# Kernel tuning notes

Hardware: AMD Instinct MI355X
Metric: run time of the kernel (lower is better)

The kernel has to match this reference:

```python
import jax, jax.numpy as jnp
import numpy as np
import math

BLOCK = 8
N_COEFF = BLOCK * BLOCK  # 64
N_SAMPLE = 250
SEED = 0  # args.seed

# zigzag order: flat index m*8+n from the hardcoded loc table
ZIGZAG = jnp.array([
    0, 1, 8, 16, 9, 2, 3, 10, 17, 24, 32, 25, 18, 11, 4, 5,
    12, 19, 26, 33, 40, 48, 41, 34, 27, 20, 13, 6, 7, 14, 21, 28,
    35, 42, 49, 56, 57, 50, 43, 36, 29, 22, 15, 23, 30, 37, 44, 51,
    58, 59, 52, 45, 38, 31, 39, 46, 53, 60, 61, 54, 47, 55, 62, 63
], dtype=jnp.int32)


def dct_matrix():
    Q = np.zeros((BLOCK, BLOCK), dtype=np.float32)
    Q[0, :] = math.sqrt(1.0 / BLOCK)
    for i in range(1, BLOCK):
        for j in range(BLOCK):
            Q[i, j] = math.sqrt(2.0 / BLOCK) * math.cos((2 * j + 1) * math.pi * i / (2.0 * BLOCK))
    return jnp.asarray(Q)


def setup_inputs() -> dict:
    key = jax.random.key(0)
    x = jax.random.uniform(key, (64, 3, 512, 512), dtype=jnp.float32)
    return {"x": x}


def reference(x):
    Q = dct_matrix()
    # rgb -> ycbcr, luminance channel only (module discards Cb/Cr)
    x255 = x * 255.0
    y = (0.299 * x255[:, 0] + 0.587 * x255[:, 1] + 0.114 * x255[:, 2]) / 255.0  # [B,H,W]
    B, H, W = y.shape
    a, b = H // BLOCK, W // BLOCK
    # split into 8x8 blocks: [B, a, b, 8, 8]
    blocks = y.reshape(B, a, BLOCK, b, BLOCK).transpose(0, 1, 3, 2, 4)
    # per-block 2D DCT: Q @ block @ Q^T, batched as one einsum
    dct = jnp.einsum('ij,nabjk,lk->nabil', Q, blocks, Q)  # [B,a,b,8,8]
    image_dct_result = dct.transpose(0, 1, 3, 2, 4).reshape(B, 1, H, W)
    # zigzag gather over flattened block coefficients -> [B, 64, a*b]
    dist = dct.reshape(B, a * b, N_COEFF)[:, :, ZIGZAG].transpose(0, 2, 1)
    # per (sample, coefficient) random permutation sampling of 250 blocks
    keys = jax.random.split(jax.random.key(SEED), B * N_COEFF)
    idx = jax.vmap(lambda k: jax.random.permutation(k, a * b)[:N_SAMPLE])(keys)
    idx = idx.reshape(B, N_COEFF, N_SAMPLE)
    dct_coeff_sample = jnp.take_along_axis(dist, idx, axis=2)  # [B,64,250]
    return image_dct_result, dct_coeff_sample
```

## Files before the change

kernel.cpp:

```cpp
#include <hip/hip_runtime.h>
#include <hip/hip_bf16.h>
#include <cstdint>


#define BATCH 64
#define HW 512
#define NBLK 4096
#define NSAMPLE 250
#define IMG_ELEMS (HW * HW)

#define A0 0.35355339059327373f
#define A1 0.49039264020161522f
#define A2 0.46193976625564337f
#define A3 0.41573480615127262f
#define A4 0.35355339059327379f
#define A5 0.27778511650980111f
#define A6 0.19134171618254492f
#define A7 0.09754516100806412f

__constant__ float Qc[8][8] = {
    { A0,  A0,  A0,  A0,  A0,  A0,  A0,  A0},
    { A1,  A3,  A5,  A7, -A7, -A5, -A3, -A1},
    { A2,  A6, -A6, -A2, -A2, -A6,  A6,  A2},
    { A3, -A7, -A1, -A5,  A5,  A1,  A7, -A3},
    { A4, -A4, -A4,  A4,  A4, -A4, -A4,  A4},
    { A5, -A1,  A7,  A3, -A3, -A7,  A1, -A5},
    { A6, -A2,  A2, -A6, -A6,  A2, -A2,  A6},
    { A7, -A5,  A3, -A1,  A1, -A3,  A5, -A7},
};

__constant__ int ZIGZAG[64] = {
    0, 1, 8, 16, 9, 2, 3, 10, 17, 24, 32, 25, 18, 11, 4, 5,
    12, 19, 26, 33, 40, 48, 41, 34, 27, 20, 13, 6, 7, 14, 21, 28,
    35, 42, 49, 56, 57, 50, 43, 36, 29, 22, 15, 23, 30, 37, 44, 51,
    58, 59, 52, 45, 38, 31, 39, 46, 53, 60, 61, 54, 47, 55, 62, 63
};

__global__ __launch_bounds__(256) void dct_kernel(const float* __restrict__ x,
                                                  float* __restrict__ out) {
    __shared__ float ylds[8 * 8 * 32];

    const int t = threadIdx.x;
    const int wg = blockIdx.x;
    const int b = wg >> 7;
    const int ai = (wg >> 1) & 63;
    const int h = wg & 1;
    const int row0 = ai * 8;
    const int colbase = h * 256;

    {
        const int k = t >> 5;
        const int cg = t & 31;
        size_t off = (size_t)b * 3 * IMG_ELEMS + (size_t)(row0 + k) * HW +
                     colbase + cg * 8;
        float4 r0 = *(const float4*)(x + off);
        float4 r1 = *(const float4*)(x + off + 4);
        float4 g0 = *(const float4*)(x + off + IMG_ELEMS);
        float4 g1 = *(const float4*)(x + off + IMG_ELEMS + 4);
        float4 b0 = *(const float4*)(x + off + 2 * IMG_ELEMS);
        float4 b1 = *(const float4*)(x + off + 2 * IMG_ELEMS + 4);
        float R[8] = {r0.x, r0.y, r0.z, r0.w, r1.x, r1.y, r1.z, r1.w};
        float G[8] = {g0.x, g0.y, g0.z, g0.w, g1.x, g1.y, g1.z, g1.w};
        float B[8] = {b0.x, b0.y, b0.z, b0.w, b1.x, b1.y, b1.z, b1.w};
#pragma unroll
        for (int jj = 0; jj < 8; ++jj) {
            float y = (0.299f * (R[jj] * 255.0f) + 0.587f * (G[jj] * 255.0f) +
                       0.114f * (B[jj] * 255.0f)) / 255.0f;
            ylds[k * 256 + jj * 32 + cg] = y;
        }
    }
    __syncthreads();

    const int i = t >> 5;
    const int bi = t & 31;
    float qrow[8];
#pragma unroll
    for (int k = 0; k < 8; ++k) qrow[k] = Qc[i][k];

    float acc[8];
#pragma unroll
    for (int j = 0; j < 8; ++j) acc[j] = 0.0f;
#pragma unroll
    for (int k = 0; k < 8; ++k) {
#pragma unroll
        for (int j = 0; j < 8; ++j)
            acc[j] += qrow[k] * ylds[k * 256 + j * 32 + bi];
    }

    float d[8];
#pragma unroll
    for (int j = 0; j < 8; ++j) {
        float s = 0.0f;
#pragma unroll
        for (int k = 0; k < 8; ++k) s += acc[k] * Qc[j][k];
        d[j] = s;
    }
    float4* o = (float4*)(out + (size_t)b * IMG_ELEMS +
                          (size_t)(row0 + i) * HW + colbase + bi * 8);
    o[0] = make_float4(d[0], d[1], d[2], d[3]);
    o[1] = make_float4(d[4], d[5], d[6], d[7]);
}

__device__ __forceinline__ uint32_t rotl32(uint32_t v, int d) {
    return (v << d) | (v >> (32 - d));
}

__device__ __forceinline__ void tf2x32(uint32_t k0, uint32_t k1,
                                       uint32_t x0, uint32_t x1,
                                       uint32_t& o0, uint32_t& o1) {
    uint32_t ks0 = k0, ks1 = k1, ks2 = k0 ^ k1 ^ 0x1BD11BDAu;
    x0 += ks0; x1 += ks1;
#define TF_R(r) { x0 += x1; x1 = rotl32(x1, r); x1 ^= x0; }
    TF_R(13) TF_R(15) TF_R(26) TF_R(6)
    x0 += ks1; x1 += ks2 + 1u;
    TF_R(17) TF_R(29) TF_R(16) TF_R(24)
    x0 += ks2; x1 += ks0 + 2u;
    TF_R(13) TF_R(15) TF_R(26) TF_R(6)
    x0 += ks0; x1 += ks1 + 3u;
    TF_R(17) TF_R(29) TF_R(16) TF_R(24)
    x0 += ks1; x1 += ks2 + 4u;
    TF_R(13) TF_R(15) TF_R(26) TF_R(6)
    x0 += ks2; x1 += ks0 + 5u;
#undef TF_R
    o0 = x0; o1 = x1;
}

__device__ __forceinline__ void build4096(
    uint32_t s0, uint32_t s1,
    uint32_t* __restrict__ pack32, uint32_t* __restrict__ hist32,
    int tid, int w, int lane, uint32_t* __restrict__ wsum) {
    uint16_t* hist16 = (uint16_t*)hist32;

    __syncthreads();
#pragma unroll
    for (int q = 0; q < 4; ++q) hist32[tid + q * 512] = 0u;
    uint32_t keys[8];
#pragma unroll
    for (int e = 0; e < 8; ++e) {
        uint32_t o0, o1;
        tf2x32(s0, s1, 0u, (uint32_t)(tid + e * 512), o0, o1);
        keys[e] = o0 ^ o1;
    }
    __syncthreads();

    uint32_t ord[8];
#pragma unroll
    for (int e = 0; e < 8; ++e) {
        uint32_t bkt = keys[e] >> 20;
        uint32_t sh = (bkt & 1) << 4;
        uint32_t old = atomicAdd(&hist32[bkt >> 1], 1u << sh);
        ord[e] = (old >> sh) & 0xFFFFu;
    }
    __syncthreads();

    uint4 wv = ((const uint4*)hist32)[tid];
    uint32_t c0 = wv.x & 0xFFFFu, c1 = wv.x >> 16;
    uint32_t c2 = wv.y & 0xFFFFu, c3 = wv.y >> 16;
    uint32_t c4 = wv.z & 0xFFFFu, c5 = wv.z >> 16;
    uint32_t c6 = wv.w & 0xFFFFu, c7 = wv.w >> 16;
    uint32_t ssum = c0 + c1 + c2 + c3 + c4 + c5 + c6 + c7;
    uint32_t sc = ssum;
#pragma unroll
    for (int off = 1; off < 64; off <<= 1) {
        uint32_t t = __shfl_up(sc, off);
        if (lane >= off) sc += t;
    }
    if (lane == 63) wsum[w] = sc;
    __syncthreads();
    uint32_t ex = sc - ssum;
    for (int ww = 0; ww < w; ++ww) ex += wsum[ww];
    uint32_t p1 = ex + c0, p2 = p1 + c1, p3 = p2 + c2, p4 = p3 + c3;
    uint32_t p5 = p4 + c4, p6 = p5 + c5, p7 = p6 + c6, p8 = p7 + c7;
    uint4 ov;
    ov.x = p1 | (p2 << 16); ov.y = p3 | (p4 << 16);
    ov.z = p5 | (p6 << 16); ov.w = p7 | (p8 << 16);
    ((uint4*)hist32)[tid] = ov;
    __syncthreads();

#pragma unroll
    for (int e = 0; e < 8; ++e) {
        uint32_t bkt = keys[e] >> 20;
        uint32_t start = bkt ? (uint32_t)hist16[bkt - 1] : 0u;
        pack32[start + ord[e]] =
            ((keys[e] & 0xFFFFFu) << 12) | (uint32_t)(tid + e * 512);
    }
}

__device__ __forceinline__ uint32_t select4096(
    const uint16_t* __restrict__ hist16, const uint32_t* __restrict__ pack32,
    uint32_t s) {
    uint32_t lo = 0, hi = 4095;
#pragma unroll
    for (int it = 0; it < 12; ++it) {
        uint32_t mid = (lo + hi) >> 1;
        if ((uint32_t)hist16[mid] > s) hi = mid; else lo = mid + 1;
    }
    uint32_t b = lo;
    uint32_t start = b ? (uint32_t)hist16[b - 1] : 0u;
    uint32_t L = (uint32_t)hist16[b] - start;
    uint32_t c = pack32[start];
    if (L > 1) {
        uint32_t k = s - start;
        for (uint32_t cand = 0; cand < L; ++cand) {
            uint32_t cc = pack32[start + cand];
            uint32_t cnt = 0;
            for (uint32_t o = 0; o < L; ++o)
                cnt += (pack32[start + o] < cc) ? 1u : 0u;
            if (cnt == k) { c = cc; break; }
        }
    }
    return c & 0xFFFu;
}

__global__ __launch_bounds__(512) void sample_kernel(const float* __restrict__ img,
                                                     float* __restrict__ out2) {
    __shared__ __align__(16) uint32_t pack32[NBLK];
    __shared__ __align__(16) uint32_t hist32[2048];
    __shared__ uint16_t jsel[256];
    __shared__ uint32_t wsum[8];
    uint16_t* hist16 = (uint16_t*)hist32;

    const int tid = threadIdx.x;
    const int w = tid >> 6;
    const int lane = tid & 63;
    const int gb = blockIdx.x;

    uint32_t k0, k1, n0, n1, sA0, sA1, sB0, sB1;
    tf2x32(0u, 0u, 0u, (uint32_t)gb, k0, k1);
    tf2x32(k0, k1, 0u, 0u, n0, n1);
    tf2x32(k0, k1, 0u, 1u, sA0, sA1);
    tf2x32(n0, n1, 0u, 1u, sB0, sB1);

    build4096(sB0, sB1, pack32, hist32, tid, w, lane, wsum);
    __syncthreads();
    if (tid < NSAMPLE)
        jsel[tid] = (uint16_t)select4096(hist16, pack32, (uint32_t)tid);

    build4096(sA0, sA1, pack32, hist32, tid, w, lane, wsum);
    __syncthreads();

    int b = gb >> 6, c = gb & 63;
    int z = ZIGZAG[c];
    int i0z = z >> 3, j0z = z & 7;
    if (tid < NSAMPLE) {
        uint32_t i = select4096(hist16, pack32, (uint32_t)jsel[tid]);
        int ai = (int)i >> 6, bi = (int)i & 63;
        out2[(size_t)gb * NSAMPLE + tid] =
            img[(size_t)b * IMG_ELEMS + (size_t)(ai * 8 + i0z) * HW +
                (bi * 8 + j0z)];
    }
}

extern "C" void kernel_launch(void* const* d_in, const int* in_sizes, int n_in,
                              void* d_out, int out_size, void* d_ws, size_t ws_size,
                              hipStream_t stream) {
    const float* x = (const float*)d_in[0];
    float* out = (float*)d_out;
    dct_kernel<<<BATCH * 128, 256, 0, stream>>>(x, out);
    sample_kernel<<<BATCH * 64, 512, 0, stream>>>(out, out + (size_t)BATCH * IMG_ELEMS);
}
```

Measured before the change: 392.0 us.

## Interleave DCT and permutation-index work in one kernel, gather samples afterward

The DCT work and the random-permutation index computation now run side by side in one launch: odd workgroups do two DCT tiles each and even workgroups do the sampling-index build. Sampled indices go to a workspace buffer, and a small gather kernel then reads the DCT output. The point is to overlap the memory-bound DCT with the compute-bound Threefry/sort work, so the index generation no longer waits for the DCT to finish. In exchange it adds a workspace round trip and a third dependent step, and the DCT blocks carry a larger shared-memory footprint.

```diff
diff --git a/kernel.cpp b/kernel.cpp
--- a/kernel.cpp
+++ b/kernel.cpp
@@ -35,71 +35,6 @@
     35, 42, 49, 56, 57, 50, 43, 36, 29, 22, 15, 23, 30, 37, 44, 51,
     58, 59, 52, 45, 38, 31, 39, 46, 53, 60, 61, 54, 47, 55, 62, 63
 };
-
-__global__ __launch_bounds__(256) void dct_kernel(const float* __restrict__ x,
-                                                  float* __restrict__ out) {
-    __shared__ float ylds[8 * 8 * 32];
-
-    const int t = threadIdx.x;
-    const int wg = blockIdx.x;
-    const int b = wg >> 7;
-    const int ai = (wg >> 1) & 63;
-    const int h = wg & 1;
-    const int row0 = ai * 8;
-    const int colbase = h * 256;
-
-    {
-        const int k = t >> 5;
-        const int cg = t & 31;
-        size_t off = (size_t)b * 3 * IMG_ELEMS + (size_t)(row0 + k) * HW +
-                     colbase + cg * 8;
-        float4 r0 = *(const float4*)(x + off);
-        float4 r1 = *(const float4*)(x + off + 4);
-        float4 g0 = *(const float4*)(x + off + IMG_ELEMS);
-        float4 g1 = *(const float4*)(x + off + IMG_ELEMS + 4);
-        float4 b0 = *(const float4*)(x + off + 2 * IMG_ELEMS);
-        float4 b1 = *(const float4*)(x + off + 2 * IMG_ELEMS + 4);
-        float R[8] = {r0.x, r0.y, r0.z, r0.w, r1.x, r1.y, r1.z, r1.w};
-        float G[8] = {g0.x, g0.y, g0.z, g0.w, g1.x, g1.y, g1.z, g1.w};
-        float B[8] = {b0.x, b0.y, b0.z, b0.w, b1.x, b1.y, b1.z, b1.w};
-#pragma unroll
-        for (int jj = 0; jj < 8; ++jj) {
-            float y = (0.299f * (R[jj] * 255.0f) + 0.587f * (G[jj] * 255.0f) +
-                       0.114f * (B[jj] * 255.0f)) / 255.0f;
-            ylds[k * 256 + jj * 32 + cg] = y;
-        }
-    }
-    __syncthreads();
-
-    const int i = t >> 5;
-    const int bi = t & 31;
-    float qrow[8];
-#pragma unroll
-    for (int k = 0; k < 8; ++k) qrow[k] = Qc[i][k];
-
-    float acc[8];
-#pragma unroll
-    for (int j = 0; j < 8; ++j) acc[j] = 0.0f;
-#pragma unroll
-    for (int k = 0; k < 8; ++k) {
-#pragma unroll
-        for (int j = 0; j < 8; ++j)
-            acc[j] += qrow[k] * ylds[k * 256 + j * 32 + bi];
-    }
-
-    float d[8];
-#pragma unroll
-    for (int j = 0; j < 8; ++j) {
-        float s = 0.0f;
-#pragma unroll
-        for (int k = 0; k < 8; ++k) s += acc[k] * Qc[j][k];
-        d[j] = s;
-    }
-    float4* o = (float4*)(out + (size_t)b * IMG_ELEMS +
-                          (size_t)(row0 + i) * HW + colbase + bi * 8);
-    o[0] = make_float4(d[0], d[1], d[2], d[3]);
-    o[1] = make_float4(d[4], d[5], d[6], d[7]);
-}
 
 __device__ __forceinline__ uint32_t rotl32(uint32_t v, int d) {
     return (v << d) | (v >> (32 - d));
@@ -212,43 +147,119 @@
     return c & 0xFFFu;
 }
 
-__global__ __launch_bounds__(512) void sample_kernel(const float* __restrict__ img,
-                                                     float* __restrict__ out2) {
-    __shared__ __align__(16) uint32_t pack32[NBLK];
-    __shared__ __align__(16) uint32_t hist32[2048];
-    __shared__ uint16_t jsel[256];
+__global__ __launch_bounds__(512) void fused_kernel(const float* __restrict__ x,
+                                                    float* __restrict__ out,
+                                                    uint32_t* __restrict__ ws) {
+    __shared__ __align__(16) uint8_t smem[25088];
     __shared__ uint32_t wsum[8];
-    uint16_t* hist16 = (uint16_t*)hist32;
 
     const int tid = threadIdx.x;
-    const int w = tid >> 6;
-    const int lane = tid & 63;
+
+    if (blockIdx.x & 1) {
+        float* ylds = (float*)smem + (tid >> 8) * 2048;
+        const int t = tid & 255;
+        const int wg = ((int)blockIdx.x & ~1) | (tid >> 8);
+        const int b = wg >> 7;
+        const int ai = (wg >> 1) & 63;
+        const int h = wg & 1;
+        const int row0 = ai * 8;
+        const int colbase = h * 256;
+
+        {
+            const int k = t >> 5;
+            const int cg = t & 31;
+            size_t off = (size_t)b * 3 * IMG_ELEMS + (size_t)(row0 + k) * HW +
+                         colbase + cg * 8;
+            float4 r0 = *(const float4*)(x + off);
+            float4 r1 = *(const float4*)(x + off + 4);
+            float4 g0 = *(const float4*)(x + off + IMG_ELEMS);
+            float4 g1 = *(const float4*)(x + off + IMG_ELEMS + 4);
+            float4 b0 = *(const float4*)(x + off + 2 * IMG_ELEMS);
+            float4 b1 = *(const float4*)(x + off + 2 * IMG_ELEMS + 4);
+            float R[8] = {r0.x, r0.y, r0.z, r0.w, r1.x, r1.y, r1.z, r1.w};
+            float G[8] = {g0.x, g0.y, g0.z, g0.w, g1.x, g1.y, g1.z, g1.w};
+            float B[8] = {b0.x, b0.y, b0.z, b0.w, b1.x, b1.y, b1.z, b1.w};
+#pragma unroll
+            for (int jj = 0; jj < 8; ++jj) {
+                float y = (0.299f * (R[jj] * 255.0f) + 0.587f * (G[jj] * 255.0f) +
+                           0.114f * (B[jj] * 255.0f)) / 255.0f;
+                ylds[k * 256 + jj * 32 + cg] = y;
+            }
+        }
+        __syncthreads();
+
+        const int i = t >> 5;
+        const int bi = t & 31;
+        float qrow[8];
+#pragma unroll
+        for (int k = 0; k < 8; ++k) qrow[k] = Qc[i][k];
+
+        float acc[8];
+#pragma unroll
+        for (int j = 0; j < 8; ++j) acc[j] = 0.0f;
+#pragma unroll
+        for (int k = 0; k < 8; ++k) {
+#pragma unroll
+            for (int j = 0; j < 8; ++j)
+                acc[j] += qrow[k] * ylds[k * 256 + j * 32 + bi];
+        }
+
+        float d[8];
+#pragma unroll
+        for (int j = 0; j < 8; ++j) {
+            float s = 0.0f;
+#pragma unroll
+            for (int k = 0; k < 8; ++k) s += acc[k] * Qc[j][k];
+            d[j] = s;
+        }
+        float4* o = (float4*)(out + (size_t)b * IMG_ELEMS +
+                              (size_t)(row0 + i) * HW + colbase + bi * 8);
+        o[0] = make_float4(d[0], d[1], d[2], d[3]);
+        o[1] = make_float4(d[4], d[5], d[6], d[7]);
+    } else {
+        uint32_t* pack32 = (uint32_t*)smem;
+        uint32_t* hist32 = (uint32_t*)(smem + 16384);
+        uint16_t* jsel = (uint16_t*)(smem + 24576);
+        uint16_t* hist16 = (uint16_t*)hist32;
+
+        const int w = tid >> 6;
+        const int lane = tid & 63;
+        const int gb = (int)blockIdx.x >> 1;
+
+        uint32_t k0, k1, n0, n1, sA0, sA1, sB0, sB1;
+        tf2x32(0u, 0u, 0u, (uint32_t)gb, k0, k1);
+        tf2x32(k0, k1, 0u, 0u, n0, n1);
+        tf2x32(k0, k1, 0u, 1u, sA0, sA1);
+        tf2x32(n0, n1, 0u, 1u, sB0, sB1);
+
+        build4096(sB0, sB1, pack32, hist32, tid, w, lane, wsum);
+        __syncthreads();
+        if (tid < NSAMPLE)
+            jsel[tid] = (uint16_t)select4096(hist16, pack32, (uint32_t)tid);
+
+        build4096(sA0, sA1, pack32, hist32, tid, w, lane, wsum);
+        __syncthreads();
+
+        int b = gb >> 6, c = gb & 63;
+        int z = ZIGZAG[c];
+        int i0z = z >> 3, j0z = z & 7;
+        if (tid < NSAMPLE) {
+            uint32_t i = select4096(hist16, pack32, (uint32_t)jsel[tid]);
+            int ai = (int)i >> 6, bi = (int)i & 63;
+            ws[(size_t)gb * 256 + tid] =
+                (uint32_t)((size_t)b * IMG_ELEMS +
+                           (size_t)(ai * 8 + i0z) * HW + (bi * 8 + j0z));
+        }
+    }
+}
+
+__global__ __launch_bounds__(256) void gather_kernel(
+    const float* __restrict__ img, const uint32_t* __restrict__ ws,
+    float* __restrict__ out2) {
     const int gb = blockIdx.x;
-
-    uint32_t k0, k1, n0, n1, sA0, sA1, sB0, sB1;
-    tf2x32(0u, 0u, 0u, (uint32_t)gb, k0, k1);
-    tf2x32(k0, k1, 0u, 0u, n0, n1);
-    tf2x32(k0, k1, 0u, 1u, sA0, sA1);
-    tf2x32(n0, n1, 0u, 1u, sB0, sB1);
-
-    build4096(sB0, sB1, pack32, hist32, tid, w, lane, wsum);
-    __syncthreads();
-    if (tid < NSAMPLE)
-        jsel[tid] = (uint16_t)select4096(hist16, pack32, (uint32_t)tid);
-
-    build4096(sA0, sA1, pack32, hist32, tid, w, lane, wsum);
-    __syncthreads();
-
-    int b = gb >> 6, c = gb & 63;
-    int z = ZIGZAG[c];
-    int i0z = z >> 3, j0z = z & 7;
-    if (tid < NSAMPLE) {
-        uint32_t i = select4096(hist16, pack32, (uint32_t)jsel[tid]);
-        int ai = (int)i >> 6, bi = (int)i & 63;
-        out2[(size_t)gb * NSAMPLE + tid] =
-            img[(size_t)b * IMG_ELEMS + (size_t)(ai * 8 + i0z) * HW +
-                (bi * 8 + j0z)];
-    }
+    const int s = threadIdx.x;
+    if (s < NSAMPLE)
+        out2[(size_t)gb * NSAMPLE + s] = img[ws[(size_t)gb * 256 + s]];
 }
 
 extern "C" void kernel_launch(void* const* d_in, const int* in_sizes, int n_in,
@@ -256,6 +267,8 @@
                               hipStream_t stream) {
     const float* x = (const float*)d_in[0];
     float* out = (float*)d_out;
-    dct_kernel<<<BATCH * 128, 256, 0, stream>>>(x, out);
-    sample_kernel<<<BATCH * 64, 512, 0, stream>>>(out, out + (size_t)BATCH * IMG_ELEMS);
-}
+    uint32_t* ws = (uint32_t*)d_ws;
+    fused_kernel<<<BATCH * 128, 512, 0, stream>>>(x, out, ws);
+    gather_kernel<<<BATCH * 64, 256, 0, stream>>>(
+        out, ws, out + (size_t)BATCH * IMG_ELEMS);
+}
```

Result: slower. 422.4 us (+7.8%).
